# Kernel tuning notes

Measured on AMD Instinct MI355X. Metric: run time of the kernel, lower is better.

## Reference

```python
import jax, jax.numpy as jnp
import numpy as np

N, E, D, H, G = 50000, 800000, 128, 128, 64
EPS = 1e-5


def setup_inputs() -> dict:
    key = jax.random.key(0)
    ks = jax.random.split(key, 16)
    x = jax.random.normal(ks[0], (N, D), dtype=jnp.float32)
    edge_index = jax.random.randint(ks[1], (2, E), 0, N, dtype=jnp.int64)
    batch = jnp.sort(jax.random.randint(ks[2], (N,), 0, G, dtype=jnp.int64))
    dims = [D, H, H, H]
    params = {}
    for i in range(3):
        params[f"W{i}"] = jax.random.normal(ks[3 + i], (dims[i], dims[i + 1]), dtype=jnp.float32) * (1.0 / np.sqrt(dims[i]).astype(np.float32))
        params[f"b{i}"] = jnp.zeros((dims[i + 1],), jnp.float32)
        params[f"g{i}"] = jnp.ones((dims[i + 1],), jnp.float32)   # BN gamma
        params[f"be{i}"] = jnp.zeros((dims[i + 1],), jnp.float32)  # BN beta
    params["Wout"] = jax.random.normal(ks[10], (H, 1), dtype=jnp.float32) * (1.0 / np.sqrt(H).astype(np.float32))
    params["bout"] = jnp.zeros((1,), jnp.float32)
    return {"x": x, "edge_index": edge_index, "batch": batch, **params}


def _gcn_forward(x, edge_index, batch, Ws, bs, gs, bes, Wout, bout):
    n = x.shape[0]
    loop = jnp.arange(n)
    # GCNConv default: add self-loops, symmetric degree normalization
    src = jnp.concatenate([edge_index[0], loop])
    dst = jnp.concatenate([edge_index[1], loop])
    deg = jax.ops.segment_sum(jnp.ones_like(dst, x.dtype), dst, num_segments=n)
    dinv = jax.lax.rsqrt(jnp.maximum(deg, 1.0))  # deg >= 1 from self-loops
    norm = dinv[src] * dinv[dst]                 # [E+N]
    h = x
    for W, b, g, be in zip(Ws, bs, gs, bes):
        h = h @ W                                               # transform [N,C]
        msg = h[src] * norm[:, None]                            # gather [E+N,C]
        h = jax.ops.segment_sum(msg, dst, num_segments=n) + b   # scatter-add
        # BatchNorm1d (training-mode batch statistics over nodes)
        mu = jnp.mean(h, axis=0)
        var = jnp.var(h, axis=0)
        h = (h - mu) * jax.lax.rsqrt(var + EPS) * g + be
        h = jax.nn.relu(h)
        # dropout: identity (deterministic eval reference)
    counts = jax.ops.segment_sum(jnp.ones((n,), h.dtype), batch, num_segments=G)
    pooled = jax.ops.segment_sum(h, batch, num_segments=G) / jnp.maximum(counts, 1.0)[:, None]
    return jax.nn.sigmoid(pooled @ Wout + bout)  # [G,1]


def reference(x, edge_index, batch, W0, b0, g0, be0, W1, b1, g1, be1, W2, b2, g2, be2, Wout, bout):
    return _gcn_forward(x, edge_index, batch,
                        (W0, W1, W2), (b0, b1, b2), (g0, g1, g2), (be0, be1, be2),
                        Wout, bout)
```

## Files before the change

### kernel.cpp

```cpp
#include <hip/hip_runtime.h>

#define EPSBN 1e-5f
#define AGG_BLOCKS 2048

using bf16x8 = __attribute__((ext_vector_type(8))) short;
using f32x4  = __attribute__((ext_vector_type(4))) float;

__device__ __forceinline__ unsigned short f2bf(float f) {
    unsigned u = __builtin_bit_cast(unsigned, f);
    unsigned r = (u + 0x7FFFu + ((u >> 16) & 1u)) >> 16;
    return (unsigned short)r;
}
__device__ __forceinline__ float bf2f(unsigned short s) {
    unsigned u = ((unsigned)s) << 16;
    return __builtin_bit_cast(float, u);
}


__global__ __launch_bounds__(256) void k_bhist(const int* __restrict__ dst, int E,
                                               int* __restrict__ deg, int* __restrict__ bcnt, int shift) {
    __shared__ int lh[512];
    for (int i = threadIdx.x; i < 512; i += 256) lh[i] = 0;
    __syncthreads();
    for (int i = blockIdx.x * blockDim.x + threadIdx.x; i < E; i += gridDim.x * blockDim.x) {
        int d = dst[i];
        atomicAdd(&deg[d], 1);
        atomicAdd(&lh[d >> shift], 1);
    }
    __syncthreads();
    for (int i = threadIdx.x; i < 512; i += 256)
        if (lh[i]) atomicAdd(&bcnt[i], lh[i]);
}

__global__ void k_dinv(const int* __restrict__ deg, int N, float* __restrict__ dinv) {
    int i = blockIdx.x * blockDim.x + threadIdx.x;
    if (i < N) dinv[i] = rsqrtf((float)(deg[i] + 1));
}

__global__ void k_scan1(const int* __restrict__ deg, int N, int* __restrict__ rs, int* __restrict__ blk) {
    __shared__ int sh[256];
    int tid = threadIdx.x;
    int i = blockIdx.x * 256 + tid;
    int v = (i < N) ? deg[i] : 0;
    sh[tid] = v; __syncthreads();
    for (int off = 1; off < 256; off <<= 1) {
        int t = (tid >= off) ? sh[tid - off] : 0;
        __syncthreads();
        sh[tid] += t;
        __syncthreads();
    }
    if (i < N) rs[i] = sh[tid] - v;
    if (tid == 255) blk[blockIdx.x] = sh[255];
}

__global__ void k_scan2(const int* __restrict__ blk, int nb, int* __restrict__ blkoff) {
    __shared__ int sh[1024];
    int tid = threadIdx.x;
    int v = (tid < nb) ? blk[tid] : 0;
    sh[tid] = v; __syncthreads();
    for (int off = 1; off < 1024; off <<= 1) {
        int t = (tid >= off) ? sh[tid - off] : 0;
        __syncthreads();
        sh[tid] += t;
        __syncthreads();
    }
    if (tid < nb) blkoff[tid] = sh[tid] - v;
}

__global__ void k_scan3(int* __restrict__ rs, int N, const int* __restrict__ blkoff) {
    int i = blockIdx.x * blockDim.x + threadIdx.x;
    if (i < N) rs[i] += blkoff[i >> 8];
}


__global__ __launch_bounds__(256) void k_bscatter(const int* __restrict__ src, const int* __restrict__ dst, int E,
                                                  const int* __restrict__ boff, int* __restrict__ gcur,
                                                  uint2* __restrict__ ebuf, int shift) {
    __shared__ int lh[512], lb[512];
    int tid = threadIdx.x;
    int base = blockIdx.x * 2048;
    for (int i = tid; i < 512; i += 256) lh[i] = 0;
    __syncthreads();
    int ms[8], md[8];
    #pragma unroll
    for (int j = 0; j < 8; ++j) {
        int idx = base + j * 256 + tid;
        if (idx < E) {
            ms[j] = src[idx]; md[j] = dst[idx];
            atomicAdd(&lh[md[j] >> shift], 1);
        } else md[j] = -1;
    }
    __syncthreads();
    for (int b = tid; b < 512; b += 256) {
        int c = lh[b];
        lb[b] = c ? atomicAdd(&gcur[b], c) : 0;
    }
    __syncthreads();
    for (int i = tid; i < 512; i += 256) lh[i] = 0;
    __syncthreads();
    #pragma unroll
    for (int j = 0; j < 8; ++j) {
        if (md[j] >= 0) {
            int b = md[j] >> shift;
            int r = atomicAdd(&lh[b], 1);
            ebuf[boff[b] + lb[b] + r] = make_uint2((unsigned)ms[j], (unsigned)md[j]);
        }
    }
}


__global__ __launch_bounds__(256) void k_fill2(const uint2* __restrict__ ebuf, const int* __restrict__ bcnt,
                                               const int* __restrict__ boff, const int* __restrict__ rs,
                                               const float* __restrict__ dinv,
                                               uint2* __restrict__ colw, int shift) {
    __shared__ int lcur[256];
    int b = blockIdx.x;
    int n0 = b << shift;
    int cnt = bcnt[b], s = boff[b];
    int span = 1 << shift;
    for (int i = threadIdx.x; i < span; i += 256) lcur[i] = 0;
    __syncthreads();
    for (int i = threadIdx.x; i < cnt; i += 256) {
        uint2 e = ebuf[s + i];
        int d = (int)e.y;
        int sv = (int)e.x;
        int pos = rs[d] + atomicAdd(&lcur[d - n0], 1);
        colw[pos] = make_uint2((unsigned)sv, __builtin_bit_cast(unsigned, dinv[sv]));
    }
}


__global__ __launch_bounds__(256) void k_wprep(const float* __restrict__ W0, const float* __restrict__ W1,
                                               const float* __restrict__ W2, unsigned short* __restrict__ Wimg) {
    const float* W = (blockIdx.x == 0) ? W0 : (blockIdx.x == 1) ? W1 : W2;
    unsigned short* out = Wimg + (size_t)blockIdx.x * 16384;
    int tid = threadIdx.x;
    int n = tid & 127, kh = tid >> 7;
    const float* wp = &W[(kh * 64) * 128 + n];
    #pragma unroll
    for (int kb = 0; kb < 8; ++kb) {
        unsigned short t8[8];
        #pragma unroll
        for (int e = 0; e < 8; ++e)
            t8[e] = f2bf(wp[(kb * 8 + e) * 128]);
        int byte = (n * 256 + kh * 128 + kb * 16) ^ ((n & 7) << 4);
        *reinterpret_cast<uint4*>(reinterpret_cast<char*>(out) + byte) =
            *reinterpret_cast<const uint4*>(t8);
    }
}


__global__ __launch_bounds__(256) void k_gemm(const unsigned short* __restrict__ Abf,
                                              const float* __restrict__ Af,
                                              const unsigned short* __restrict__ Wimg,
                                              unsigned short* __restrict__ C, int N,
                                              const float* __restrict__ scale,
                                              const float* __restrict__ shift, int mode) {
    __shared__ unsigned short Asw[128 * 128];
    __shared__ unsigned short Wt[128 * 128];
    int tid = threadIdx.x;
    int r0 = blockIdx.x * 128;

    {
        const uint4* wi = reinterpret_cast<const uint4*>(Wimg);
        uint4* wl = reinterpret_cast<uint4*>(Wt);
        #pragma unroll
        for (int j = 0; j < 8; ++j)
            wl[tid + j * 256] = wi[tid + j * 256];
    }
    if (mode == 0) {
        const float* ap = &Af[(size_t)r0 * 128];
        #pragma unroll
        for (int j = 0; j < 8; ++j) {
            int u = tid + j * 256;
            int row = u >> 4, cg = u & 15;
            unsigned short t8[8] = {0,0,0,0,0,0,0,0};
            if (r0 + row < N) {
                float4 a0 = *reinterpret_cast<const float4*>(ap + row * 128 + cg * 8);
                float4 a1 = *reinterpret_cast<const float4*>(ap + row * 128 + cg * 8 + 4);
                t8[0]=f2bf(a0.x); t8[1]=f2bf(a0.y); t8[2]=f2bf(a0.z); t8[3]=f2bf(a0.w);
                t8[4]=f2bf(a1.x); t8[5]=f2bf(a1.y); t8[6]=f2bf(a1.z); t8[7]=f2bf(a1.w);
            }
            int byte = (row * 256 + cg * 16) ^ ((row & 7) << 4);
            *reinterpret_cast<uint4*>(reinterpret_cast<char*>(Asw) + byte) =
                *reinterpret_cast<const uint4*>(t8);
        }
    } else {
        const unsigned short* ap = &Abf[(size_t)r0 * 128];
        #pragma unroll
        for (int j = 0; j < 8; ++j) {
            int u = tid + j * 256;
            int row = u >> 4, cg = u & 15;
            unsigned short t8[8] = {0,0,0,0,0,0,0,0};
            if (r0 + row < N) {
                ushort4 v0 = *reinterpret_cast<const ushort4*>(ap + (size_t)row * 128 + cg * 8);
                ushort4 v1 = *reinterpret_cast<const ushort4*>(ap + (size_t)row * 128 + cg * 8 + 4);
                float4 sc0 = *reinterpret_cast<const float4*>(&scale[cg * 8]);
                float4 sc1 = *reinterpret_cast<const float4*>(&scale[cg * 8 + 4]);
                float4 sf0 = *reinterpret_cast<const float4*>(&shift[cg * 8]);
                float4 sf1 = *reinterpret_cast<const float4*>(&shift[cg * 8 + 4]);
                t8[0] = f2bf(fmaxf(bf2f(v0.x) * sc0.x + sf0.x, 0.f));
                t8[1] = f2bf(fmaxf(bf2f(v0.y) * sc0.y + sf0.y, 0.f));
                t8[2] = f2bf(fmaxf(bf2f(v0.z) * sc0.z + sf0.z, 0.f));
                t8[3] = f2bf(fmaxf(bf2f(v0.w) * sc0.w + sf0.w, 0.f));
                t8[4] = f2bf(fmaxf(bf2f(v1.x) * sc1.x + sf1.x, 0.f));
                t8[5] = f2bf(fmaxf(bf2f(v1.y) * sc1.y + sf1.y, 0.f));
                t8[6] = f2bf(fmaxf(bf2f(v1.z) * sc1.z + sf1.z, 0.f));
                t8[7] = f2bf(fmaxf(bf2f(v1.w) * sc1.w + sf1.w, 0.f));
            }
            int byte = (row * 256 + cg * 16) ^ ((row & 7) << 4);
            *reinterpret_cast<uint4*>(reinterpret_cast<char*>(Asw) + byte) =
                *reinterpret_cast<const uint4*>(t8);
        }
    }
    __syncthreads();

    int wv = tid >> 6, lane = tid & 63;
    int lr = lane & 15, lk = lane >> 4;
    f32x4 acc[2][8] = {};
    #pragma unroll
    for (int kk = 0; kk < 4; ++kk) {
        bf16x8 af[2], bf[8];
        #pragma unroll
        for (int mf = 0; mf < 2; ++mf) {
            int ar = wv * 32 + mf * 16 + lr;
            int byte = (ar * 256 + kk * 64 + lk * 16) ^ ((ar & 7) << 4);
            af[mf] = *reinterpret_cast<const bf16x8*>(reinterpret_cast<const char*>(Asw) + byte);
        }
        #pragma unroll
        for (int nf = 0; nf < 8; ++nf) {
            int bn = nf * 16 + lr;
            int byte = (bn * 256 + kk * 64 + lk * 16) ^ ((bn & 7) << 4);
            bf[nf] = *reinterpret_cast<const bf16x8*>(reinterpret_cast<const char*>(Wt) + byte);
        }
        #pragma unroll
        for (int mf = 0; mf < 2; ++mf)
            #pragma unroll
            for (int nf = 0; nf < 8; ++nf)
                acc[mf][nf] = __builtin_amdgcn_mfma_f32_16x16x32_bf16(af[mf], bf[nf], acc[mf][nf], 0, 0, 0);
    }
    __syncthreads();
    #pragma unroll
    for (int mf = 0; mf < 2; ++mf)
        #pragma unroll
        for (int nf = 0; nf < 8; ++nf)
            #pragma unroll
            for (int r = 0; r < 4; ++r) {
                int row = wv * 32 + mf * 16 + lk * 4 + r;
                int colc = nf * 16 + lr;
                Asw[row * 128 + colc] = f2bf(acc[mf][nf][r]);
            }
    __syncthreads();
    #pragma unroll
    for (int j = 0; j < 8; ++j) {
        int u = tid + j * 256;
        int row = u >> 4, cg = u & 15;
        if (r0 + row < N)
            *reinterpret_cast<uint4*>(&C[((size_t)(r0 + row)) * 128 + cg * 8]) =
                *reinterpret_cast<const uint4*>(&Asw[row * 128 + cg * 8]);
    }
}


__global__ __launch_bounds__(256) void k_agg(const unsigned short* __restrict__ t, const uint2* __restrict__ colw,
                                             const int* __restrict__ rs, const int* __restrict__ deg,
                                             const float* __restrict__ dinv, const float* __restrict__ bias,
                                             unsigned short* __restrict__ out, int N,
                                             float* __restrict__ p1, float* __restrict__ p2) {
    __shared__ uint2 ec[4][64];
    __shared__ float sh[4][64][4];
    int wv = threadIdx.x >> 6, lane = threadIdx.x & 63;
    const ushort2* tp = reinterpret_cast<const ushort2*>(t);
    float b0 = bias[2 * lane], b1 = bias[2 * lane + 1];
    float s1x = 0.f, s1y = 0.f, s2x = 0.f, s2y = 0.f;
    for (int w = blockIdx.x * 4 + wv; w < N; w += gridDim.x * 4) {
        int start = rs[w], cnt = deg[w];
        float di = dinv[w];
        float ax = 0.f, ay = 0.f;
        for (int base = 0; base < cnt; base += 64) {
            int m = min(cnt - base, 64);
            if (lane < m) ec[wv][lane] = colw[start + base + lane];
            asm volatile("s_waitcnt lgkmcnt(0)" ::: "memory");
            int e = 0;
            for (; e + 4 <= m; e += 4) {
                uint2 e0 = ec[wv][e], e1 = ec[wv][e + 1], e2 = ec[wv][e + 2], e3 = ec[wv][e + 3];
                ushort2 v0 = tp[(size_t)e0.x * 64 + lane];
                ushort2 v1 = tp[(size_t)e1.x * 64 + lane];
                ushort2 v2 = tp[(size_t)e2.x * 64 + lane];
                ushort2 v3 = tp[(size_t)e3.x * 64 + lane];
                float w0 = __builtin_bit_cast(float, e0.y), w1 = __builtin_bit_cast(float, e1.y);
                float w2 = __builtin_bit_cast(float, e2.y), w3 = __builtin_bit_cast(float, e3.y);
                ax += w0 * bf2f(v0.x) + w1 * bf2f(v1.x) + w2 * bf2f(v2.x) + w3 * bf2f(v3.x);
                ay += w0 * bf2f(v0.y) + w1 * bf2f(v1.y) + w2 * bf2f(v2.y) + w3 * bf2f(v3.y);
            }
            for (; e < m; ++e) {
                uint2 ee = ec[wv][e];
                ushort2 v = tp[(size_t)ee.x * 64 + lane];
                float ww = __builtin_bit_cast(float, ee.y);
                ax += ww * bf2f(v.x);
                ay += ww * bf2f(v.y);
            }
        }
        ushort2 self = tp[(size_t)w * 64 + lane];
        ushort2 o;
        o.x = f2bf(di * ax + di * di * bf2f(self.x) + b0);
        o.y = f2bf(di * ay + di * di * bf2f(self.y) + b1);
        reinterpret_cast<ushort2*>(out)[(size_t)w * 64 + lane] = o;
        float rx = bf2f(o.x), ry = bf2f(o.y);
        s1x += rx; s1y += ry; s2x += rx * rx; s2y += ry * ry;
    }
    sh[wv][lane][0] = s1x; sh[wv][lane][1] = s1y; sh[wv][lane][2] = s2x; sh[wv][lane][3] = s2y;
    __syncthreads();
    int tid = threadIdx.x;
    if (tid < 64) {
        float a0 = 0.f, a1 = 0.f, a2 = 0.f, a3 = 0.f;
        #pragma unroll
        for (int r = 0; r < 4; ++r) {
            a0 += sh[r][tid][0]; a1 += sh[r][tid][1];
            a2 += sh[r][tid][2]; a3 += sh[r][tid][3];
        }
        p1[blockIdx.x * 128 + 2 * tid]     = a0;
        p1[blockIdx.x * 128 + 2 * tid + 1] = a1;
        p2[blockIdx.x * 128 + 2 * tid]     = a2;
        p2[blockIdx.x * 128 + 2 * tid + 1] = a3;
    }
}


__global__ __launch_bounds__(128) void k_statsmid(const float* __restrict__ p1, const float* __restrict__ p2,
                                                  int rows, float* __restrict__ pm1, float* __restrict__ pm2) {
    int c = threadIdx.x, b = blockIdx.x;
    int r0 = b * rows;
    float s1 = 0.f, s2 = 0.f;
    #pragma unroll 4
    for (int r = 0; r < rows; ++r) {
        s1 += p1[(size_t)(r0 + r) * 128 + c];
        s2 += p2[(size_t)(r0 + r) * 128 + c];
    }
    pm1[b * 128 + c] = s1;
    pm2[b * 128 + c] = s2;
}

__global__ __launch_bounds__(1024) void k_stats2(const float* __restrict__ p1, const float* __restrict__ p2,
                                                 int nb, int N,
                                                 const float* __restrict__ g, const float* __restrict__ be,
                                                 float* __restrict__ scale, float* __restrict__ shift) {
    __shared__ double sh1[1024], sh2[1024];
    int tid = threadIdx.x;
    int c = tid & 127, seg = tid >> 7;
    double s1 = 0.0, s2 = 0.0;
    int b = seg;
    for (; b + 32 <= nb; b += 32) {
        double a0 = p1[(b      ) * 128 + c], q0 = p2[(b      ) * 128 + c];
        double a1 = p1[(b +  8) * 128 + c], q1 = p2[(b +  8) * 128 + c];
        double a2 = p1[(b + 16) * 128 + c], q2 = p2[(b + 16) * 128 + c];
        double a3 = p1[(b + 24) * 128 + c], q3 = p2[(b + 24) * 128 + c];
        s1 += (a0 + a1) + (a2 + a3);
        s2 += (q0 + q1) + (q2 + q3);
    }
    for (; b < nb; b += 8) { s1 += p1[b * 128 + c]; s2 += p2[b * 128 + c]; }
    sh1[tid] = s1; sh2[tid] = s2;
    __syncthreads();
    #pragma unroll
    for (int s = 4; s >= 1; s >>= 1) {
        if (seg < s) {
            sh1[tid] += sh1[tid + s * 128];
            sh2[tid] += sh2[tid + s * 128];
        }
        __syncthreads();
    }
    if (tid < 128) {
        double mu = sh1[c] / N;
        double var = sh2[c] / N - mu * mu;
        double inv = 1.0 / sqrt(var + (double)EPSBN);
        scale[c] = (float)((double)g[c] * inv);
        shift[c] = (float)((double)be[c] - mu * (double)g[c] * inv);
    }
}


__global__ __launch_bounds__(256) void k_pool(const unsigned short* __restrict__ h, const int* __restrict__ batch,
                                              const float* __restrict__ scale, const float* __restrict__ shift,
                                              const float* __restrict__ Wout, int N, int G,
                                              float* __restrict__ pool, int* __restrict__ cnt) {
    __shared__ float pl[64];
    __shared__ int cl[64];
    int tid = threadIdx.x;
    if (tid < 64) { pl[tid] = 0.f; cl[tid] = 0; }
    __syncthreads();
    int wv = tid >> 6, lane = tid & 63;
    float sc0 = scale[2 * lane], sc1 = scale[2 * lane + 1];
    float sf0 = shift[2 * lane], sf1 = shift[2 * lane + 1];
    float w0 = Wout[2 * lane], w1 = Wout[2 * lane + 1];
    const ushort2* hp = reinterpret_cast<const ushort2*>(h);
    int wid = blockIdx.x * 4 + wv;
    int stride = gridDim.x * 4;
    for (int i = wid; i < N; i += stride * 4) {
        int i1 = i + stride, i2 = i + 2 * stride, i3 = i + 3 * stride;
        float s0 = 0.f, s1 = 0.f, s2 = 0.f, s3 = 0.f;
        {
            ushort2 v = hp[(size_t)i * 64 + lane];
            s0 = fmaxf(bf2f(v.x) * sc0 + sf0, 0.f) * w0 + fmaxf(bf2f(v.y) * sc1 + sf1, 0.f) * w1;
        }
        if (i1 < N) {
            ushort2 v = hp[(size_t)i1 * 64 + lane];
            s1 = fmaxf(bf2f(v.x) * sc0 + sf0, 0.f) * w0 + fmaxf(bf2f(v.y) * sc1 + sf1, 0.f) * w1;
        }
        if (i2 < N) {
            ushort2 v = hp[(size_t)i2 * 64 + lane];
            s2 = fmaxf(bf2f(v.x) * sc0 + sf0, 0.f) * w0 + fmaxf(bf2f(v.y) * sc1 + sf1, 0.f) * w1;
        }
        if (i3 < N) {
            ushort2 v = hp[(size_t)i3 * 64 + lane];
            s3 = fmaxf(bf2f(v.x) * sc0 + sf0, 0.f) * w0 + fmaxf(bf2f(v.y) * sc1 + sf1, 0.f) * w1;
        }
        #pragma unroll
        for (int o = 32; o > 0; o >>= 1) {
            s0 += __shfl_down(s0, o); s1 += __shfl_down(s1, o);
            s2 += __shfl_down(s2, o); s3 += __shfl_down(s3, o);
        }
        if (lane == 0) {
            atomicAdd(&pl[batch[i]], s0); atomicAdd(&cl[batch[i]], 1);
            if (i1 < N) { atomicAdd(&pl[batch[i1]], s1); atomicAdd(&cl[batch[i1]], 1); }
            if (i2 < N) { atomicAdd(&pl[batch[i2]], s2); atomicAdd(&cl[batch[i2]], 1); }
            if (i3 < N) { atomicAdd(&pl[batch[i3]], s3); atomicAdd(&cl[batch[i3]], 1); }
        }
    }
    __syncthreads();
    if (tid < 64) {
        atomicAdd(&pool[tid], pl[tid]);
        atomicAdd(&cnt[tid], cl[tid]);
    }
}

__global__ void k_final(const float* __restrict__ pool, const int* __restrict__ cnt,
                        const float* __restrict__ bout, int G, float* __restrict__ out) {
    int g = blockIdx.x * blockDim.x + threadIdx.x;
    if (g < G) {
        float c = fmaxf((float)cnt[g], 1.f);
        float p = pool[g] / c + bout[0];
        out[g] = 1.f / (1.f + expf(-p));
    }
}


extern "C" void kernel_launch(void* const* d_in, const int* in_sizes, int n_in,
                              void* d_out, int out_size, void* d_ws, size_t ws_size,
                              hipStream_t stream) {
    const float* x    = (const float*)d_in[0];
    const int*   ei   = (const int*)d_in[1];
    const int*   batch= (const int*)d_in[2];
    const float* W0p  = (const float*)d_in[3];
    const float* b0p  = (const float*)d_in[4];
    const float* g0p  = (const float*)d_in[5];
    const float* be0p = (const float*)d_in[6];
    const float* W1p  = (const float*)d_in[7];
    const float* b1p  = (const float*)d_in[8];
    const float* g1p  = (const float*)d_in[9];
    const float* be1p = (const float*)d_in[10];
    const float* W2p  = (const float*)d_in[11];
    const float* b2p  = (const float*)d_in[12];
    const float* g2p  = (const float*)d_in[13];
    const float* be2p = (const float*)d_in[14];
    const float* Woutp= (const float*)d_in[15];
    const float* boutp= (const float*)d_in[16];

    int N = in_sizes[0] / 128;
    int E = in_sizes[1] / 2;
    int G = out_size;
    const int* src = ei;
    const int* dst = ei + E;

    int shiftB = 7;
    while ((((N + (1 << shiftB) - 1) >> shiftB) > 512) && shiftB < 8) ++shiftB;
    int nbuck = (N + (1 << shiftB) - 1) >> shiftB;

    char* p = (char*)d_ws;
    auto alloc = [&](size_t bytes) {
        void* q = (void*)p;
        p += (bytes + 255) & ~(size_t)255;
        return q;
    };
    unsigned short* Bt  = (unsigned short*)alloc((size_t)N * 128 * 2);
    unsigned short* Bh  = (unsigned short*)alloc((size_t)N * 128 * 2);
    uint2*  colw   = (uint2*) alloc((size_t)E * 8);
    uint2*  ebuf   = (uint2*) alloc((size_t)E * 8);
    int*    rsA    = (int*)   alloc((size_t)N * 4);
    int*    deg    = (int*)   alloc((size_t)N * 4);
    float*  dinv   = (float*) alloc((size_t)N * 4);
    int*    blk    = (int*)   alloc(1024 * 4);
    int*    blkoff = (int*)   alloc(1024 * 4);
    int*    bcnt   = (int*)   alloc(512 * 4);
    int*    boff   = (int*)   alloc(512 * 4);
    int*    gcur   = (int*)   alloc(512 * 4);
    unsigned short* Wimg = (unsigned short*)alloc(3 * 16384 * 2);
    float*  p1     = (float*) alloc((size_t)AGG_BLOCKS * 128 * 4);
    float*  p2     = (float*) alloc((size_t)AGG_BLOCKS * 128 * 4);
    float*  pm1    = (float*) alloc(128 * 128 * 4);
    float*  pm2    = (float*) alloc(128 * 128 * 4);
    float*  scale  = (float*) alloc(128 * 4);
    float*  shift  = (float*) alloc(128 * 4);
    float*  pool   = (float*) alloc(64 * 4);
    int*    cnt    = (int*)   alloc(64 * 4);

    hipMemsetAsync(deg, 0, (size_t)N * 4, stream);
    hipMemsetAsync(bcnt, 0, 512 * 4, stream);
    hipMemsetAsync(gcur, 0, 512 * 4, stream);
    hipMemsetAsync(pool, 0, 64 * 4, stream);
    hipMemsetAsync(cnt, 0, 64 * 4, stream);

    int nb = (N + 255) / 256;
    k_wprep   <<<3, 256, 0, stream>>>(W0p, W1p, W2p, Wimg);
    k_bhist   <<<256, 256, 0, stream>>>(dst, E, deg, bcnt, shiftB);
    k_dinv    <<<nb, 256, 0, stream>>>(deg, N, dinv);
    k_scan1   <<<nb, 256, 0, stream>>>(deg, N, rsA, blk);
    k_scan2   <<<1, 1024, 0, stream>>>(blk, nb, blkoff);
    k_scan3   <<<nb, 256, 0, stream>>>(rsA, N, blkoff);
    k_scan2   <<<1, 1024, 0, stream>>>(bcnt, 512, boff);
    k_bscatter<<<(E + 2047) / 2048, 256, 0, stream>>>(src, dst, E, boff, gcur, ebuf, shiftB);
    k_fill2   <<<nbuck, 256, 0, stream>>>(ebuf, bcnt, boff, rsA, dinv, colw, shiftB);

    int gemmBlocks = (N + 127) / 128;
    int midRows = AGG_BLOCKS / 128;

    k_gemm    <<<gemmBlocks, 256, 0, stream>>>(nullptr, x, Wimg, Bt, N, scale, shift, 0);
    k_agg     <<<AGG_BLOCKS, 256, 0, stream>>>(Bt, colw, rsA, deg, dinv, b0p, Bh, N, p1, p2);
    k_statsmid<<<128, 128, 0, stream>>>(p1, p2, midRows, pm1, pm2);
    k_stats2  <<<1, 1024, 0, stream>>>(pm1, pm2, 128, N, g0p, be0p, scale, shift);
    k_gemm    <<<gemmBlocks, 256, 0, stream>>>(Bh, nullptr, Wimg + 16384, Bt, N, scale, shift, 1);
    k_agg     <<<AGG_BLOCKS, 256, 0, stream>>>(Bt, colw, rsA, deg, dinv, b1p, Bh, N, p1, p2);
    k_statsmid<<<128, 128, 0, stream>>>(p1, p2, midRows, pm1, pm2);
    k_stats2  <<<1, 1024, 0, stream>>>(pm1, pm2, 128, N, g1p, be1p, scale, shift);
    k_gemm    <<<gemmBlocks, 256, 0, stream>>>(Bh, nullptr, Wimg + 32768, Bt, N, scale, shift, 1);
    k_agg     <<<AGG_BLOCKS, 256, 0, stream>>>(Bt, colw, rsA, deg, dinv, b2p, Bh, N, p1, p2);
    k_statsmid<<<128, 128, 0, stream>>>(p1, p2, midRows, pm1, pm2);
    k_stats2  <<<1, 1024, 0, stream>>>(pm1, pm2, 128, N, g2p, be2p, scale, shift);
    k_pool <<<256, 256, 0, stream>>>(Bh, batch, scale, shift, Woutp, N, G, pool, cnt);
    k_final<<<1, 64, 0, stream>>>(pool, cnt, boutp, G, (float*)d_out);
}
```

Measured before the change: 290.4 us.

## Cut kernel launches by fusing small kernels and merging memsets

Folds the dinv computation into the first scan kernel, runs both small scans in one two-block launch, and drops the intermediate stats reduction so a single 1024-thread kernel reduces all aggregation partials. The final sigmoid moves into the pooling kernel through a last-block-done atomic counter, and the five memsets become one contiguous memset. The aggregation kernel also loads the self feature before the edge loop and uses nontemporal packed stores. Fewer launches and memsets reduce launch overhead and serialization gaps, but the single-block stats kernel now reads all 2048 partial rows by itself, which may be slower than the old two-stage reduction.

```diff
diff --git a/kernel.cpp b/kernel.cpp
--- a/kernel.cpp
+++ b/kernel.cpp
@@ -32,16 +32,13 @@
         if (lh[i]) atomicAdd(&bcnt[i], lh[i]);
 }
 
-__global__ void k_dinv(const int* __restrict__ deg, int N, float* __restrict__ dinv) {
-    int i = blockIdx.x * blockDim.x + threadIdx.x;
-    if (i < N) dinv[i] = rsqrtf((float)(deg[i] + 1));
-}
-
-__global__ void k_scan1(const int* __restrict__ deg, int N, int* __restrict__ rs, int* __restrict__ blk) {
+__global__ void k_scan1(const int* __restrict__ deg, int N, int* __restrict__ rs, int* __restrict__ blk,
+                        float* __restrict__ dinv) {
     __shared__ int sh[256];
     int tid = threadIdx.x;
     int i = blockIdx.x * 256 + tid;
     int v = (i < N) ? deg[i] : 0;
+    if (i < N) dinv[i] = rsqrtf((float)(v + 1));
     sh[tid] = v; __syncthreads();
     for (int off = 1; off < 256; off <<= 1) {
         int t = (tid >= off) ? sh[tid - off] : 0;
@@ -53,10 +50,14 @@
     if (tid == 255) blk[blockIdx.x] = sh[255];
 }
 
-__global__ void k_scan2(const int* __restrict__ blk, int nb, int* __restrict__ blkoff) {
+__global__ __launch_bounds__(1024) void k_scan2x(const int* __restrict__ blk, int nb, int* __restrict__ blkoff,
+                                                 const int* __restrict__ bcnt, int nb2, int* __restrict__ boff) {
     __shared__ int sh[1024];
-    int tid = threadIdx.x;
-    int v = (tid < nb) ? blk[tid] : 0;
+    const int* in = blockIdx.x ? bcnt : blk;
+    int n = blockIdx.x ? nb2 : nb;
+    int* outp = blockIdx.x ? boff : blkoff;
+    int tid = threadIdx.x;
+    int v = (tid < n) ? in[tid] : 0;
     sh[tid] = v; __syncthreads();
     for (int off = 1; off < 1024; off <<= 1) {
         int t = (tid >= off) ? sh[tid - off] : 0;
@@ -64,7 +65,7 @@
         sh[tid] += t;
         __syncthreads();
     }
-    if (tid < nb) blkoff[tid] = sh[tid] - v;
+    if (tid < n) outp[tid] = sh[tid] - v;
 }
 
 __global__ void k_scan3(int* __restrict__ rs, int N, const int* __restrict__ blkoff) {
@@ -276,6 +277,7 @@
     for (int w = blockIdx.x * 4 + wv; w < N; w += gridDim.x * 4) {
         int start = rs[w], cnt = deg[w];
         float di = dinv[w];
+        ushort2 self = tp[(size_t)w * 64 + lane];
         float ax = 0.f, ay = 0.f;
         for (int base = 0; base < cnt; base += 64) {
             int m = min(cnt - base, 64);
@@ -301,12 +303,11 @@
                 ay += ww * bf2f(v.y);
             }
         }
-        ushort2 self = tp[(size_t)w * 64 + lane];
-        ushort2 o;
-        o.x = f2bf(di * ax + di * di * bf2f(self.x) + b0);
-        o.y = f2bf(di * ay + di * di * bf2f(self.y) + b1);
-        reinterpret_cast<ushort2*>(out)[(size_t)w * 64 + lane] = o;
-        float rx = bf2f(o.x), ry = bf2f(o.y);
+        unsigned short ox = f2bf(di * ax + di * di * bf2f(self.x) + b0);
+        unsigned short oy = f2bf(di * ay + di * di * bf2f(self.y) + b1);
+        unsigned pack = (unsigned)ox | ((unsigned)oy << 16);
+        __builtin_nontemporal_store(pack, reinterpret_cast<unsigned*>(out) + ((size_t)w * 64 + lane));
+        float rx = bf2f(ox), ry = bf2f(oy);
         s1x += rx; s1y += ry; s2x += rx * rx; s2y += ry * ry;
     }
     sh[wv][lane][0] = s1x; sh[wv][lane][1] = s1y; sh[wv][lane][2] = s2x; sh[wv][lane][3] = s2y;
@@ -319,46 +320,32 @@
             a0 += sh[r][tid][0]; a1 += sh[r][tid][1];
             a2 += sh[r][tid][2]; a3 += sh[r][tid][3];
         }
-        p1[blockIdx.x * 128 + 2 * tid]     = a0;
-        p1[blockIdx.x * 128 + 2 * tid + 1] = a1;
-        p2[blockIdx.x * 128 + 2 * tid]     = a2;
-        p2[blockIdx.x * 128 + 2 * tid + 1] = a3;
-    }
-}
-
-
-__global__ __launch_bounds__(128) void k_statsmid(const float* __restrict__ p1, const float* __restrict__ p2,
-                                                  int rows, float* __restrict__ pm1, float* __restrict__ pm2) {
-    int c = threadIdx.x, b = blockIdx.x;
-    int r0 = b * rows;
-    float s1 = 0.f, s2 = 0.f;
-    #pragma unroll 4
-    for (int r = 0; r < rows; ++r) {
-        s1 += p1[(size_t)(r0 + r) * 128 + c];
-        s2 += p2[(size_t)(r0 + r) * 128 + c];
-    }
-    pm1[b * 128 + c] = s1;
-    pm2[b * 128 + c] = s2;
-}
-
-__global__ __launch_bounds__(1024) void k_stats2(const float* __restrict__ p1, const float* __restrict__ p2,
-                                                 int nb, int N,
-                                                 const float* __restrict__ g, const float* __restrict__ be,
-                                                 float* __restrict__ scale, float* __restrict__ shift) {
+        __builtin_nontemporal_store(a0, &p1[blockIdx.x * 128 + 2 * tid]);
+        __builtin_nontemporal_store(a1, &p1[blockIdx.x * 128 + 2 * tid + 1]);
+        __builtin_nontemporal_store(a2, &p2[blockIdx.x * 128 + 2 * tid]);
+        __builtin_nontemporal_store(a3, &p2[blockIdx.x * 128 + 2 * tid + 1]);
+    }
+}
+
+
+__global__ __launch_bounds__(1024) void k_stats(const float* __restrict__ p1, const float* __restrict__ p2,
+                                                int nb, int N,
+                                                const float* __restrict__ g, const float* __restrict__ be,
+                                                float* __restrict__ scale, float* __restrict__ shift) {
     __shared__ double sh1[1024], sh2[1024];
     int tid = threadIdx.x;
     int c = tid & 127, seg = tid >> 7;
     double s1 = 0.0, s2 = 0.0;
     int b = seg;
     for (; b + 32 <= nb; b += 32) {
-        double a0 = p1[(b      ) * 128 + c], q0 = p2[(b      ) * 128 + c];
-        double a1 = p1[(b +  8) * 128 + c], q1 = p2[(b +  8) * 128 + c];
-        double a2 = p1[(b + 16) * 128 + c], q2 = p2[(b + 16) * 128 + c];
-        double a3 = p1[(b + 24) * 128 + c], q3 = p2[(b + 24) * 128 + c];
+        double a0 = p1[(size_t)(b      ) * 128 + c], q0 = p2[(size_t)(b      ) * 128 + c];
+        double a1 = p1[(size_t)(b +  8) * 128 + c], q1 = p2[(size_t)(b +  8) * 128 + c];
+        double a2 = p1[(size_t)(b + 16) * 128 + c], q2 = p2[(size_t)(b + 16) * 128 + c];
+        double a3 = p1[(size_t)(b + 24) * 128 + c], q3 = p2[(size_t)(b + 24) * 128 + c];
         s1 += (a0 + a1) + (a2 + a3);
         s2 += (q0 + q1) + (q2 + q3);
     }
-    for (; b < nb; b += 8) { s1 += p1[b * 128 + c]; s2 += p2[b * 128 + c]; }
+    for (; b < nb; b += 8) { s1 += p1[(size_t)b * 128 + c]; s2 += p2[(size_t)b * 128 + c]; }
     sh1[tid] = s1; sh2[tid] = s2;
     __syncthreads();
     #pragma unroll
@@ -381,10 +368,13 @@
 
 __global__ __launch_bounds__(256) void k_pool(const unsigned short* __restrict__ h, const int* __restrict__ batch,
                                               const float* __restrict__ scale, const float* __restrict__ shift,
-                                              const float* __restrict__ Wout, int N, int G,
-                                              float* __restrict__ pool, int* __restrict__ cnt) {
+                                              const float* __restrict__ Wout, const float* __restrict__ bout,
+                                              int N, int G, int nblocks,
+                                              float* __restrict__ pool, int* __restrict__ cnt,
+                                              int* __restrict__ done, float* __restrict__ outp) {
     __shared__ float pl[64];
     __shared__ int cl[64];
+    __shared__ int lastFlag;
     int tid = threadIdx.x;
     if (tid < 64) { pl[tid] = 0.f; cl[tid] = 0; }
     __syncthreads();
@@ -431,15 +421,18 @@
         atomicAdd(&pool[tid], pl[tid]);
         atomicAdd(&cnt[tid], cl[tid]);
     }
-}
-
-__global__ void k_final(const float* __restrict__ pool, const int* __restrict__ cnt,
-                        const float* __restrict__ bout, int G, float* __restrict__ out) {
-    int g = blockIdx.x * blockDim.x + threadIdx.x;
-    if (g < G) {
-        float c = fmaxf((float)cnt[g], 1.f);
-        float p = pool[g] / c + bout[0];
-        out[g] = 1.f / (1.f + expf(-p));
+    __threadfence();
+    if (tid == 0) {
+        int old = atomicAdd(done, 1);
+        lastFlag = (old == nblocks - 1);
+    }
+    __syncthreads();
+    if (lastFlag && tid < G) {
+        float pv = atomicAdd(&pool[tid], 0.f);
+        int cv = atomicAdd(&cnt[tid], 0);
+        float c = fmaxf((float)cv, 1.f);
+        float p = pv / c + bout[0];
+        outp[tid] = 1.f / (1.f + expf(-p));
     }
 }
 
@@ -486,55 +479,45 @@
     uint2*  colw   = (uint2*) alloc((size_t)E * 8);
     uint2*  ebuf   = (uint2*) alloc((size_t)E * 8);
     int*    rsA    = (int*)   alloc((size_t)N * 4);
-    int*    deg    = (int*)   alloc((size_t)N * 4);
     float*  dinv   = (float*) alloc((size_t)N * 4);
     int*    blk    = (int*)   alloc(1024 * 4);
     int*    blkoff = (int*)   alloc(1024 * 4);
-    int*    bcnt   = (int*)   alloc(512 * 4);
     int*    boff   = (int*)   alloc(512 * 4);
-    int*    gcur   = (int*)   alloc(512 * 4);
     unsigned short* Wimg = (unsigned short*)alloc(3 * 16384 * 2);
     float*  p1     = (float*) alloc((size_t)AGG_BLOCKS * 128 * 4);
     float*  p2     = (float*) alloc((size_t)AGG_BLOCKS * 128 * 4);
-    float*  pm1    = (float*) alloc(128 * 128 * 4);
-    float*  pm2    = (float*) alloc(128 * 128 * 4);
     float*  scale  = (float*) alloc(128 * 4);
     float*  shift  = (float*) alloc(128 * 4);
+    char*   z0     = p;
+    int*    deg    = (int*)   alloc((size_t)N * 4);
+    int*    bcnt   = (int*)   alloc(512 * 4);
+    int*    gcur   = (int*)   alloc(512 * 4);
     float*  pool   = (float*) alloc(64 * 4);
     int*    cnt    = (int*)   alloc(64 * 4);
-
-    hipMemsetAsync(deg, 0, (size_t)N * 4, stream);
-    hipMemsetAsync(bcnt, 0, 512 * 4, stream);
-    hipMemsetAsync(gcur, 0, 512 * 4, stream);
-    hipMemsetAsync(pool, 0, 64 * 4, stream);
-    hipMemsetAsync(cnt, 0, 64 * 4, stream);
+    int*    done   = (int*)   alloc(256);
+    size_t  zbytes = (size_t)(p - z0);
+
+    hipMemsetAsync(z0, 0, zbytes, stream);
 
     int nb = (N + 255) / 256;
     k_wprep   <<<3, 256, 0, stream>>>(W0p, W1p, W2p, Wimg);
     k_bhist   <<<256, 256, 0, stream>>>(dst, E, deg, bcnt, shiftB);
-    k_dinv    <<<nb, 256, 0, stream>>>(deg, N, dinv);
-    k_scan1   <<<nb, 256, 0, stream>>>(deg, N, rsA, blk);
-    k_scan2   <<<1, 1024, 0, stream>>>(blk, nb, blkoff);
+    k_scan1   <<<nb, 256, 0, stream>>>(deg, N, rsA, blk, dinv);
+    k_scan2x  <<<2, 1024, 0, stream>>>(blk, nb, blkoff, bcnt, 512, boff);
     k_scan3   <<<nb, 256, 0, stream>>>(rsA, N, blkoff);
-    k_scan2   <<<1, 1024, 0, stream>>>(bcnt, 512, boff);
     k_bscatter<<<(E + 2047) / 2048, 256, 0, stream>>>(src, dst, E, boff, gcur, ebuf, shiftB);
     k_fill2   <<<nbuck, 256, 0, stream>>>(ebuf, bcnt, boff, rsA, dinv, colw, shiftB);
 
     int gemmBlocks = (N + 127) / 128;
-    int midRows = AGG_BLOCKS / 128;
-
-    k_gemm    <<<gemmBlocks, 256, 0, stream>>>(nullptr, x, Wimg, Bt, N, scale, shift, 0);
-    k_agg     <<<AGG_BLOCKS, 256, 0, stream>>>(Bt, colw, rsA, deg, dinv, b0p, Bh, N, p1, p2);
-    k_statsmid<<<128, 128, 0, stream>>>(p1, p2, midRows, pm1, pm2);
-    k_stats2  <<<1, 1024, 0, stream>>>(pm1, pm2, 128, N, g0p, be0p, scale, shift);
-    k_gemm    <<<gemmBlocks, 256, 0, stream>>>(Bh, nullptr, Wimg + 16384, Bt, N, scale, shift, 1);
-    k_agg     <<<AGG_BLOCKS, 256, 0, stream>>>(Bt, colw, rsA, deg, dinv, b1p, Bh, N, p1, p2);
-    k_statsmid<<<128, 128, 0, stream>>>(p1, p2, midRows, pm1, pm2);
-    k_stats2  <<<1, 1024, 0, stream>>>(pm1, pm2, 128, N, g1p, be1p, scale, shift);
-    k_gemm    <<<gemmBlocks, 256, 0, stream>>>(Bh, nullptr, Wimg + 32768, Bt, N, scale, shift, 1);
-    k_agg     <<<AGG_BLOCKS, 256, 0, stream>>>(Bt, colw, rsA, deg, dinv, b2p, Bh, N, p1, p2);
-    k_statsmid<<<128, 128, 0, stream>>>(p1, p2, midRows, pm1, pm2);
-    k_stats2  <<<1, 1024, 0, stream>>>(pm1, pm2, 128, N, g2p, be2p, scale, shift);
-    k_pool <<<256, 256, 0, stream>>>(Bh, batch, scale, shift, Woutp, N, G, pool, cnt);
-    k_final<<<1, 64, 0, stream>>>(pool, cnt, boutp, G, (float*)d_out);
-}
+
+    k_gemm <<<gemmBlocks, 256, 0, stream>>>(nullptr, x, Wimg, Bt, N, scale, shift, 0);
+    k_agg  <<<AGG_BLOCKS, 256, 0, stream>>>(Bt, colw, rsA, deg, dinv, b0p, Bh, N, p1, p2);
+    k_stats<<<1, 1024, 0, stream>>>(p1, p2, AGG_BLOCKS, N, g0p, be0p, scale, shift);
+    k_gemm <<<gemmBlocks, 256, 0, stream>>>(Bh, nullptr, Wimg + 16384, Bt, N, scale, shift, 1);
+    k_agg  <<<AGG_BLOCKS, 256, 0, stream>>>(Bt, colw, rsA, deg, dinv, b1p, Bh, N, p1, p2);
+    k_stats<<<1, 1024, 0, stream>>>(p1, p2, AGG_BLOCKS, N, g1p, be1p, scale, shift);
+    k_gemm <<<gemmBlocks, 256, 0, stream>>>(Bh, nullptr, Wimg + 32768, Bt, N, scale, shift, 1);
+    k_agg  <<<AGG_BLOCKS, 256, 0, stream>>>(Bt, colw, rsA, deg, dinv, b2p, Bh, N, p1, p2);
+    k_stats<<<1, 1024, 0, stream>>>(p1, p2, AGG_BLOCKS, N, g2p, be2p, scale, shift);
+    k_pool <<<256, 256, 0, stream>>>(Bh, batch, scale, shift, Woutp, boutp, N, G, 256, pool, cnt, done, (float*)d_out);
+}
```

After: 409.8 us. 41.1% more time.
